# Kernel tuning notes

Hardware: AMD Instinct MI355X
Metric: run time of the kernel (lower is better)

## Reference

```python
import jax, jax.numpy as jnp
import numpy as np

PATCH = 16
HIDDEN = 1024
NUM_HEADS = 16
HEAD_DIM = HIDDEN // NUM_HEADS


def sinusoidal_pe(n, d):
    # standard transformer sinusoidal positional encoding, shape [n, d]
    pos = np.arange(n, dtype=np.float32)[:, None]
    i = np.arange(0, d, 2, dtype=np.float32)[None, :]
    ang = pos / np.power(10000.0, i / d)
    pe = np.zeros((n, d), dtype=np.float32)
    pe[:, 0::2] = np.sin(ang)
    pe[:, 1::2] = np.cos(ang)
    return jnp.asarray(pe)


def patch_embed(x, w, b):
    # Conv2d(kernel=stride=PATCH) == non-overlapping patch GEMM
    B, C, H, W = x.shape
    hp, wp = H // PATCH, W // PATCH
    xp = x.reshape(B, C, hp, PATCH, wp, PATCH)
    t = jnp.einsum('bchpwq,dcpq->bhwd', xp, w)  # [B, hp, wp, D]
    return t.reshape(B, hp * wp, -1) + b        # [B, N, D]


def _fit(x, w, b):
    t = patch_embed(x, w, b)
    t = t + sinusoidal_pe(t.shape[1], t.shape[2])
    B, N, _ = t.shape
    return t.reshape(B, N, NUM_HEADS, HEAD_DIM).transpose(0, 2, 1, 3)  # [B,H,N,hd]


def setup_inputs() -> dict:
    key = jax.random.key(0)
    ks = jax.random.split(key, 9)
    B, C, H, W = 16, 3, 512, 512
    return {
        'q_img': jax.random.normal(ks[0], (B, C, H, W), jnp.float32),
        'k_img': jax.random.normal(ks[1], (B, C, H, W), jnp.float32),
        'v_img': jax.random.normal(ks[2], (B, C, H, W), jnp.float32),
        'wq': jax.random.normal(ks[3], (HIDDEN, C, PATCH, PATCH), jnp.float32) * 0.02,
        'bq': jax.random.normal(ks[4], (HIDDEN,), jnp.float32) * 0.02,
        'wk': jax.random.normal(ks[5], (HIDDEN, C, PATCH, PATCH), jnp.float32) * 0.02,
        'bk': jax.random.normal(ks[6], (HIDDEN,), jnp.float32) * 0.02,
        'wv': jax.random.normal(ks[7], (HIDDEN, C, PATCH, PATCH), jnp.float32) * 0.02,
        'bv': jax.random.normal(ks[8], (HIDDEN,), jnp.float32) * 0.02,
    }


def reference(q_img, k_img, v_img, wq, bq, wk, bk, wv, bv):
    q = _fit(q_img, wq, bq)  # [B,H,N,hd]
    k = _fit(k_img, wk, bk)
    v = _fit(v_img, wv, bv)
    q = jax.nn.softmax(q, axis=-1)   # softmax over head_dim
    k = jax.nn.softmax(k, axis=-2)   # softmax over tokens
    scores = jnp.einsum('bhnd,bhne->bhde', k, v)   # k^T v : [B,H,hd,hd]
    ctx = jnp.einsum('bhnd,bhde->bhne', q, scores)  # [B,H,N,hd]
    B, h, N, hd = ctx.shape
    return ctx.transpose(0, 2, 1, 3).reshape(B, N, h * hd)  # [B,N,hidden]
```

## Files before the change

kernel.cpp:

```cpp
#include <hip/hip_runtime.h>
#include <hip/hip_bf16.h>


typedef float  f32x4  __attribute__((ext_vector_type(4)));
typedef __bf16 bf16x8 __attribute__((ext_vector_type(8)));
typedef __bf16 bf16x4 __attribute__((ext_vector_type(4)));

#define LN10000 9.210340371976184f

__device__ __forceinline__ unsigned short f2bf_bits(float f){
  union { float f; unsigned u; } a; a.f = f;
  unsigned r = a.u + 0x7FFFu + ((a.u >> 16) & 1u);
  return (unsigned short)(r >> 16);
}

__device__ __forceinline__ void gload16(const void* g, void* l){
  __builtin_amdgcn_global_load_lds((__attribute__((address_space(1))) void*)g,
                                   (__attribute__((address_space(3))) void*)l,
                                   16, 0, 0);
}


__global__ __launch_bounds__(256) void k_prep_w(
    const float* __restrict__ wq, const float* __restrict__ wk,
    const float* __restrict__ wv, unsigned short* __restrict__ wbf)
{
  int i = blockIdx.x*256 + threadIdx.x;
  if (i >= 589824) return;
  int z = i / 196608;
  int r = i - z*196608;
  const float* src = (z==0) ? wq : (z==1 ? wk : wv);
  f32x4 v = ((const f32x4*)src)[r];
  unsigned lo = (unsigned)f2bf_bits(v[0]) | ((unsigned)f2bf_bits(v[1]) << 16);
  unsigned hh = (unsigned)f2bf_bits(v[2]) | ((unsigned)f2bf_bits(v[3]) << 16);
  ((uint2*)wbf)[i] = make_uint2(lo, hh);
}

__global__ __launch_bounds__(256) void k_prep_pe(float* __restrict__ pe)
{
  int i = blockIdx.x*256 + threadIdx.x;
  if (i >= 1048576) return;
  int n = i >> 10, dd = i & 1023;
  float ex  = (float)(dd & ~1) * (1.0f/1024.0f);
  float ang = (float)n * expf(-LN10000 * ex);
  pe[i] = (dd & 1) ? cosf(ang) : sinf(ang);
}


__global__ __launch_bounds__(256, 2) void k_embed(
    const float* __restrict__ xq, const float* __restrict__ xk,
    const float* __restrict__ xv, const unsigned short* __restrict__ wbf,
    const float* __restrict__ bq, const float* __restrict__ bk,
    const float* __restrict__ bv, const float* __restrict__ pe,
    unsigned short* __restrict__ t_bf)
{
  __shared__ __align__(16) float          ldsA[128*64];
  __shared__ __align__(16) unsigned short ldsB[128*64];

  const int tid = threadIdx.x;
  int flat = blockIdx.x + (blockIdx.y << 3) + (blockIdx.z << 10);
  int orig = (flat & 7)*384 + (flat >> 3);
  const int z   = orig >> 10;
  const int rem = orig & 1023;
  const int m0  = (rem >> 3) * 128;
  const int d0  = (rem & 7) * 128;

  const float* x = (z==0) ? xq : (z==1 ? xk : xv);
  const unsigned short* wz = wbf + z*786432;
  const float* bias = (z==0) ? bq : (z==1 ? bk : bv);
  unsigned short* tout = t_bf + (size_t)z*16777216u;

  int aRow[8], aKK[8];
#pragma unroll
  for (int i=0;i<8;i++){
    int L   = i*4096 + tid*16;
    int row = L >> 8;
    int U   = L ^ ((row & 7) << 4);
    aKK[i]  = (U >> 2) & 63;
    int m   = m0 + row;
    int bimg = m >> 10, nt = m & 1023;
    aRow[i] = bimg*786432 + (nt>>5)*8192 + (nt&31)*16;
  }
  int bOff[4];
#pragma unroll
  for (int i=0;i<4;i++){
    int L   = i*4096 + tid*16;
    int row = L >> 7;
    int U   = L ^ ((row & 7) << 4);
    bOff[i] = (d0 + row)*768 + ((U >> 1) & 63);
  }

  const int lane = tid & 63;
  const int wid  = tid >> 6;
  const int ln   = lane & 15, hi4 = lane >> 4;
  const int wm   = wid >> 1,  wn  = wid & 1;

  f32x4 acc[4][4] = {};
  char* ldsAc = (char*)ldsA;
  char* ldsBc = (char*)ldsB;

  for (int ks=0; ks<12; ++ks){
#pragma unroll
    for (int i=0;i<8;i++){
      int k   = ks*64 + aKK[i];
      int c   = k >> 8, rem2 = k & 255;
      int goff = aRow[i] + c*262144 + (rem2>>4)*512 + (rem2 & 15);
      gload16(x + goff, ldsAc + i*4096 + wid*1024);
    }
#pragma unroll
    for (int i=0;i<4;i++){
      gload16(wz + bOff[i] + ks*64, ldsBc + i*4096 + wid*1024);
    }
    __syncthreads();

#pragma unroll
    for (int kc=0; kc<2; ++kc){
      bf16x8 af[4], bfr[4];
#pragma unroll
      for (int mi=0;mi<4;mi++){
        int row  = wm*64 + mi*16 + ln;
        int swz  = (row & 7) << 4;
        int base = row*256 + kc*128 + hi4*32;
        f32x4 lo = *(const f32x4*)(ldsAc + ( base        ^ swz));
        f32x4 hh = *(const f32x4*)(ldsAc + ((base + 16)  ^ swz));
        bf16x8 t;
        t[0]=(__bf16)lo[0]; t[1]=(__bf16)lo[1]; t[2]=(__bf16)lo[2]; t[3]=(__bf16)lo[3];
        t[4]=(__bf16)hh[0]; t[5]=(__bf16)hh[1]; t[6]=(__bf16)hh[2]; t[7]=(__bf16)hh[3];
        af[mi] = t;
      }
#pragma unroll
      for (int ni=0;ni<4;ni++){
        int row  = wn*64 + ni*16 + ln;
        int swz  = (row & 7) << 4;
        int base = row*128 + kc*64 + hi4*16;
        bfr[ni] = *(const bf16x8*)(ldsBc + (base ^ swz));
      }
#pragma unroll
      for (int mi=0;mi<4;mi++)
#pragma unroll
        for (int ni=0;ni<4;ni++)
          acc[mi][ni] = __builtin_amdgcn_mfma_f32_16x16x32_bf16(
              af[mi], bfr[ni], acc[mi][ni], 0, 0, 0);
    }
    __syncthreads();
  }

  float bias4[4];
#pragma unroll
  for (int ni=0;ni<4;ni++) bias4[ni] = bias[d0 + wn*64 + ni*16 + ln];

#pragma unroll
  for (int mi=0;mi<4;mi++){
#pragma unroll
    for (int r=0;r<4;r++){
      int m    = m0 + wm*64 + mi*16 + hi4*4 + r;
      int ntok = m & 1023;
      float vv[4];
#pragma unroll
      for (int ni=0;ni<4;ni++){
        int dd = d0 + wn*64 + ni*16 + ln;
        vv[ni] = acc[mi][ni][r] + bias4[ni] + pe[ntok*1024 + dd];
      }
      size_t base = (size_t)m*1024 + d0 + wn*64 + ln;
      if (z == 0){
        float ex0=__expf(vv[0]), ex1=__expf(vv[1]),
              ex2=__expf(vv[2]), ex3=__expf(vv[3]);
        float ps = ex0+ex1+ex2+ex3;
        ps += __shfl_xor(ps, 1); ps += __shfl_xor(ps, 2);
        ps += __shfl_xor(ps, 4); ps += __shfl_xor(ps, 8);
        float w = 1.0f / ps;
        tout[base +  0] = f2bf_bits(ex0*w);  tout[base + 16] = f2bf_bits(ex1*w);
        tout[base + 32] = f2bf_bits(ex2*w);  tout[base + 48] = f2bf_bits(ex3*w);
      } else if (z == 1){
        tout[base +  0] = f2bf_bits(__expf(vv[0]));
        tout[base + 16] = f2bf_bits(__expf(vv[1]));
        tout[base + 32] = f2bf_bits(__expf(vv[2]));
        tout[base + 48] = f2bf_bits(__expf(vv[3]));
      } else {
        tout[base +  0] = f2bf_bits(vv[0]); tout[base + 16] = f2bf_bits(vv[1]);
        tout[base + 32] = f2bf_bits(vv[2]); tout[base + 48] = f2bf_bits(vv[3]);
      }
    }
  }
}


__global__ __launch_bounds__(512) void k_scores(
    const __bf16* __restrict__ t_bf, float* __restrict__ scoresOut)
{
  __shared__ __align__(16) float lds[4][4096];
  __shared__ float ksumLds[8][64];

  const int tid = threadIdx.x;
  const int bh  = blockIdx.x;
  const int b   = bh >> 4, h = bh & 15;
  const __bf16* kbase = t_bf + 16777216u + (size_t)b*1048576u + h*64;
  const __bf16* vbase = t_bf + 33554432u + (size_t)b*1048576u + h*64;

  const int dq = tid & 15, eg = (tid>>4) & 3, npart = tid >> 6;
  const int srow = tid >> 3;
  const int dcol = (tid & 7) * 8;

#define STAGE(BUF, CH) do{                                                \
    size_t g = (size_t)((CH)*64 + srow)*1024 + dcol;                      \
    bf16x8 k8 = *(const bf16x8*)(kbase + g);                              \
    bf16x8 v8 = *(const bf16x8*)(vbase + g);                              \
    f32x4 e0, e1, w0, w1;                                                 \
    e0[0]=(float)k8[0]; e0[1]=(float)k8[1]; e0[2]=(float)k8[2]; e0[3]=(float)k8[3]; \
    e1[0]=(float)k8[4]; e1[1]=(float)k8[5]; e1[2]=(float)k8[6]; e1[3]=(float)k8[7]; \
    w0[0]=(float)v8[0]; w0[1]=(float)v8[1]; w0[2]=(float)v8[2]; w0[3]=(float)v8[3]; \
    w1[0]=(float)v8[4]; w1[1]=(float)v8[5]; w1[2]=(float)v8[6]; w1[3]=(float)v8[7]; \
    *(f32x4*)(&lds[BUF][srow*64 + dcol])       = e0;                      \
    *(f32x4*)(&lds[BUF][srow*64 + dcol + 4])   = e1;                      \
    *(f32x4*)(&lds[2+(BUF)][srow*64 + dcol])     = w0;                    \
    *(f32x4*)(&lds[2+(BUF)][srow*64 + dcol + 4]) = w1;                    \
  }while(0)

  float acc[4][16] = {};
  float kp[4] = {0.f,0.f,0.f,0.f};

  STAGE(0, 0);
  __syncthreads();
  for (int ch=0; ch<16; ++ch){
    int cur = ch & 1;
    if (ch < 15) STAGE(cur^1, ch+1);
    for (int nn = npart; nn < 64; nn += 8){
      f32x4 ek4 = *(const f32x4*)(&lds[cur][nn*64 + dq*4]);
      f32x4 v0  = *(const f32x4*)(&lds[2+cur][nn*64 + eg*16 + 0]);
      f32x4 v1  = *(const f32x4*)(&lds[2+cur][nn*64 + eg*16 + 4]);
      f32x4 v2  = *(const f32x4*)(&lds[2+cur][nn*64 + eg*16 + 8]);
      f32x4 v3  = *(const f32x4*)(&lds[2+cur][nn*64 + eg*16 + 12]);
#pragma unroll
      for (int i2=0;i2<4;i2++){
        kp[i2] += ek4[i2];
#pragma unroll
        for (int j=0;j<4;j++){
          acc[i2][j+0]  += ek4[i2]*v0[j];
          acc[i2][j+4]  += ek4[i2]*v1[j];
          acc[i2][j+8]  += ek4[i2]*v2[j];
          acc[i2][j+12] += ek4[i2]*v3[j];
        }
      }
    }
    __syncthreads();
  }
#undef STAGE

  if (eg == 0){
#pragma unroll
    for (int i2=0;i2<4;i2++) ksumLds[npart][dq*4 + i2] = kp[i2];
  }

  if (npart < 4){
    float* pb = &lds[npart][0];
#pragma unroll
    for (int i2=0;i2<4;i2++){
      int base = (dq*4 + i2)*64 + eg*16;
      f32x4 a0; a0[0]=acc[i2][0];  a0[1]=acc[i2][1];  a0[2]=acc[i2][2];  a0[3]=acc[i2][3];
      f32x4 a1; a1[0]=acc[i2][4];  a1[1]=acc[i2][5];  a1[2]=acc[i2][6];  a1[3]=acc[i2][7];
      f32x4 a2; a2[0]=acc[i2][8];  a2[1]=acc[i2][9];  a2[2]=acc[i2][10]; a2[3]=acc[i2][11];
      f32x4 a3; a3[0]=acc[i2][12]; a3[1]=acc[i2][13]; a3[2]=acc[i2][14]; a3[3]=acc[i2][15];
      *(f32x4*)(pb + base + 0)  = a0;
      *(f32x4*)(pb + base + 4)  = a1;
      *(f32x4*)(pb + base + 8)  = a2;
      *(f32x4*)(pb + base + 12) = a3;
    }
  }
  __syncthreads();
  if (npart >= 4){
    float* pb = &lds[npart-4][0];
#pragma unroll
    for (int i2=0;i2<4;i2++){
      int base = (dq*4 + i2)*64 + eg*16;
#pragma unroll
      for (int q=0;q<4;q++){
        f32x4 cu = *(const f32x4*)(pb + base + 4*q);
        cu[0]+=acc[i2][4*q+0]; cu[1]+=acc[i2][4*q+1];
        cu[2]+=acc[i2][4*q+2]; cu[3]+=acc[i2][4*q+3];
        *(f32x4*)(pb + base + 4*q) = cu;
      }
    }
  }
  __syncthreads();

  float* outp = scoresOut + (size_t)bh*4096;
#pragma unroll
  for (int i=0;i<2;i++){
    int idx = tid + 512*i;
    int q4  = idx*4;
    int d   = idx >> 4;
    float rk = 1.0f / (ksumLds[0][d]+ksumLds[1][d]+ksumLds[2][d]+ksumLds[3][d]
                      +ksumLds[4][d]+ksumLds[5][d]+ksumLds[6][d]+ksumLds[7][d]);
    f32x4 s = *(const f32x4*)(&lds[0][q4]) + *(const f32x4*)(&lds[1][q4])
            + *(const f32x4*)(&lds[2][q4]) + *(const f32x4*)(&lds[3][q4]);
    s[0]*=rk; s[1]*=rk; s[2]*=rk; s[3]*=rk;
    *(f32x4*)(outp + q4) = s;
  }
}


__global__ __launch_bounds__(256) void k_ctx(
    const __bf16* __restrict__ t_bf, const float* __restrict__ scoresIn,
    float* __restrict__ out)
{
  __shared__ __align__(16) float S[64*64];
  __shared__ __align__(16) float qnT[64*132];

  const int tid   = threadIdx.x;
  const int bh    = blockIdx.y;
  const int b     = bh >> 4, h = bh & 15;
  const int chunk = blockIdx.x;
  const __bf16* qbase = t_bf + (size_t)b*1048576u + h*64;

#pragma unroll
  for (int i=0;i<4;i++){
    int q4 = (tid + 256*i)*4;
    *(f32x4*)(S + q4) = *(const f32x4*)(scoresIn + (size_t)bh*4096 + q4);
  }

  const int lane = tid & 63, w = tid >> 6;
  const int pos = lane & 15, rq = lane >> 4;
#pragma unroll
  for (int p=0;p<8;p++){
    int nl = w*32 + p*4 + rq;
    int n  = chunk*128 + nl;
    bf16x4 qv = *(const bf16x4*)(qbase + (size_t)n*1024 + pos*4);
    qnT[(pos*4+0)*132 + nl] = (float)qv[0];
    qnT[(pos*4+1)*132 + nl] = (float)qv[1];
    qnT[(pos*4+2)*132 + nl] = (float)qv[2];
    qnT[(pos*4+3)*132 + nl] = (float)qv[3];
  }
  __syncthreads();

  const int eq = tid & 15, tg = tid >> 4;
  float acc[8][4] = {};
  for (int d=0; d<64; ++d){
    f32x4 s4 = *(const f32x4*)(S   + d*64  + eq*4);
    f32x4 q0 = *(const f32x4*)(qnT + d*132 + tg*8 + 0);
    f32x4 q1 = *(const f32x4*)(qnT + d*132 + tg*8 + 4);
#pragma unroll
    for (int j=0;j<4;j++){
      acc[0][j] += q0[0]*s4[j];
      acc[1][j] += q0[1]*s4[j];
      acc[2][j] += q0[2]*s4[j];
      acc[3][j] += q0[3]*s4[j];
      acc[4][j] += q1[0]*s4[j];
      acc[5][j] += q1[1]*s4[j];
      acc[6][j] += q1[2]*s4[j];
      acc[7][j] += q1[3]*s4[j];
    }
  }
#pragma unroll
  for (int i2=0;i2<8;i2++){
    int n = chunk*128 + tg*8 + i2;
    f32x4 o; o[0]=acc[i2][0]; o[1]=acc[i2][1]; o[2]=acc[i2][2]; o[3]=acc[i2][3];
    *(f32x4*)(out + (size_t)(b*1024 + n)*1024 + h*64 + eq*4) = o;
  }
}


extern "C" void kernel_launch(void* const* d_in, const int* in_sizes, int n_in,
                              void* d_out, int out_size, void* d_ws, size_t ws_size,
                              hipStream_t stream)
{
  const float* q_img = (const float*)d_in[0];
  const float* k_img = (const float*)d_in[1];
  const float* v_img = (const float*)d_in[2];
  const float* wq    = (const float*)d_in[3];
  const float* bq    = (const float*)d_in[4];
  const float* wk    = (const float*)d_in[5];
  const float* bk    = (const float*)d_in[6];
  const float* wv    = (const float*)d_in[7];
  const float* bv    = (const float*)d_in[8];
  float* out = (float*)d_out;
  char*  ws  = (char*)d_ws;

  unsigned short* t_bf   = (unsigned short*)ws;
  unsigned short* wbf    = (unsigned short*)(ws + 0x6000000);
  float*          pe     = (float*)(ws + 0x6480000);
  float*          scores = (float*)(ws + 0x6880000);

  k_prep_w <<<dim3(2304), dim3(256), 0, stream>>>(wq, wk, wv, wbf);
  k_prep_pe<<<dim3(4096), dim3(256), 0, stream>>>(pe);
  k_embed  <<<dim3(8,128,3), dim3(256), 0, stream>>>(q_img,k_img,v_img, wbf,
                                                     bq,bk,bv, pe, t_bf);
  k_scores <<<dim3(256),  dim3(512), 0, stream>>>((const __bf16*)t_bf, scores);
  k_ctx    <<<dim3(8,256), dim3(256), 0, stream>>>((const __bf16*)t_bf, scores, out);
}
```

Measured before the change: 252.1 us.

## Pre-convert input images to bf16 in a separate pass before patch-embed GEMM

Adds a k_prep_x kernel that converts the three fp32 input images to bf16 in the workspace. The embed GEMM then loads bf16 A tiles directly, which halves its A-tile LDS footprint and removes the per-fragment fp32-to-bf16 conversion. Occupancy is raised to 5 blocks per CU. The cost is an extra full read and write pass over the images (about 150MB of traffic) plus one more kernel launch.

```diff
diff --git a/kernel.cpp b/kernel.cpp
--- a/kernel.cpp
+++ b/kernel.cpp
@@ -46,15 +46,34 @@
   pe[i] = (dd & 1) ? cosf(ang) : sinf(ang);
 }
 
-
-__global__ __launch_bounds__(256, 2) void k_embed(
+__global__ __launch_bounds__(256) void k_prep_x(
     const float* __restrict__ xq, const float* __restrict__ xk,
-    const float* __restrict__ xv, const unsigned short* __restrict__ wbf,
+    const float* __restrict__ xv, unsigned short* __restrict__ x_bf)
+{
+  int i = blockIdx.x*256 + threadIdx.x;
+  if (i >= 4718592) return;
+  int z = i / 1572864;
+  int r = i - z*1572864;
+  const float* src = (z==0) ? xq : (z==1 ? xk : xv);
+  f32x4 a = ((const f32x4*)src)[r*2];
+  f32x4 b = ((const f32x4*)src)[r*2+1];
+  uint4 o;
+  o.x = (unsigned)f2bf_bits(a[0]) | ((unsigned)f2bf_bits(a[1]) << 16);
+  o.y = (unsigned)f2bf_bits(a[2]) | ((unsigned)f2bf_bits(a[3]) << 16);
+  o.z = (unsigned)f2bf_bits(b[0]) | ((unsigned)f2bf_bits(b[1]) << 16);
+  o.w = (unsigned)f2bf_bits(b[2]) | ((unsigned)f2bf_bits(b[3]) << 16);
+  ((uint4*)x_bf)[i] = o;
+}
+
+
+__global__ __launch_bounds__(256, 5) void k_embed(
+    const unsigned short* __restrict__ x_bf,
+    const unsigned short* __restrict__ wbf,
     const float* __restrict__ bq, const float* __restrict__ bk,
     const float* __restrict__ bv, const float* __restrict__ pe,
     unsigned short* __restrict__ t_bf)
 {
-  __shared__ __align__(16) float          ldsA[128*64];
+  __shared__ __align__(16) unsigned short ldsA[128*64];
   __shared__ __align__(16) unsigned short ldsB[128*64];
 
   const int tid = threadIdx.x;
@@ -65,21 +84,21 @@
   const int m0  = (rem >> 3) * 128;
   const int d0  = (rem & 7) * 128;
 
-  const float* x = (z==0) ? xq : (z==1 ? xk : xv);
-  const unsigned short* wz = wbf + z*786432;
+  const unsigned short* xbz = x_bf + (size_t)z*12582912u;
+  const unsigned short* wz  = wbf + z*786432;
   const float* bias = (z==0) ? bq : (z==1 ? bk : bv);
   unsigned short* tout = t_bf + (size_t)z*16777216u;
 
-  int aRow[8], aKK[8];
-#pragma unroll
-  for (int i=0;i<8;i++){
+  int aRowG[4], aKK[4];
+#pragma unroll
+  for (int i=0;i<4;i++){
     int L   = i*4096 + tid*16;
-    int row = L >> 8;
+    int row = L >> 7;
     int U   = L ^ ((row & 7) << 4);
-    aKK[i]  = (U >> 2) & 63;
+    aKK[i]  = (U & 127) >> 1;
     int m   = m0 + row;
     int bimg = m >> 10, nt = m & 1023;
-    aRow[i] = bimg*786432 + (nt>>5)*8192 + (nt&31)*16;
+    aRowG[i] = bimg*786432 + (nt>>5)*8192 + (nt&31)*16;
   }
   int bOff[4];
 #pragma unroll
@@ -101,11 +120,11 @@
 
   for (int ks=0; ks<12; ++ks){
 #pragma unroll
-    for (int i=0;i<8;i++){
+    for (int i=0;i<4;i++){
       int k   = ks*64 + aKK[i];
-      int c   = k >> 8, rem2 = k & 255;
-      int goff = aRow[i] + c*262144 + (rem2>>4)*512 + (rem2 & 15);
-      gload16(x + goff, ldsAc + i*4096 + wid*1024);
+      int c   = k >> 8, r2 = k & 255;
+      gload16(xbz + aRowG[i] + c*262144 + (r2>>4)*512 + (r2 & 15),
+              ldsAc + i*4096 + wid*1024);
     }
 #pragma unroll
     for (int i=0;i<4;i++){
@@ -119,21 +138,14 @@
 #pragma unroll
       for (int mi=0;mi<4;mi++){
         int row  = wm*64 + mi*16 + ln;
-        int swz  = (row & 7) << 4;
-        int base = row*256 + kc*128 + hi4*32;
-        f32x4 lo = *(const f32x4*)(ldsAc + ( base        ^ swz));
-        f32x4 hh = *(const f32x4*)(ldsAc + ((base + 16)  ^ swz));
-        bf16x8 t;
-        t[0]=(__bf16)lo[0]; t[1]=(__bf16)lo[1]; t[2]=(__bf16)lo[2]; t[3]=(__bf16)lo[3];
-        t[4]=(__bf16)hh[0]; t[5]=(__bf16)hh[1]; t[6]=(__bf16)hh[2]; t[7]=(__bf16)hh[3];
-        af[mi] = t;
+        int byte = (row*128 + kc*64 + hi4*16) ^ ((row & 7) << 4);
+        af[mi] = *(const bf16x8*)(ldsAc + byte);
       }
 #pragma unroll
       for (int ni=0;ni<4;ni++){
         int row  = wn*64 + ni*16 + ln;
-        int swz  = (row & 7) << 4;
-        int base = row*128 + kc*64 + hi4*16;
-        bfr[ni] = *(const bf16x8*)(ldsBc + (base ^ swz));
+        int byte = (row*128 + kc*64 + hi4*16) ^ ((row & 7) << 4);
+        bfr[ni] = *(const bf16x8*)(ldsBc + byte);
       }
 #pragma unroll
       for (int mi=0;mi<4;mi++)
@@ -379,10 +391,12 @@
   unsigned short* wbf    = (unsigned short*)(ws + 0x6000000);
   float*          pe     = (float*)(ws + 0x6480000);
   float*          scores = (float*)(ws + 0x6880000);
-
-  k_prep_w <<<dim3(2304), dim3(256), 0, stream>>>(wq, wk, wv, wbf);
-  k_prep_pe<<<dim3(4096), dim3(256), 0, stream>>>(pe);
-  k_embed  <<<dim3(8,128,3), dim3(256), 0, stream>>>(q_img,k_img,v_img, wbf,
+  unsigned short* x_bf   = (unsigned short*)(ws + 0x6C80000);
+
+  k_prep_w <<<dim3(2304),  dim3(256), 0, stream>>>(wq, wk, wv, wbf);
+  k_prep_pe<<<dim3(4096),  dim3(256), 0, stream>>>(pe);
+  k_prep_x <<<dim3(18432), dim3(256), 0, stream>>>(q_img, k_img, v_img, x_bf);
+  k_embed  <<<dim3(8,128,3), dim3(256), 0, stream>>>(x_bf, wbf,
                                                      bq,bk,bv, pe, t_bf);
   k_scores <<<dim3(256),  dim3(512), 0, stream>>>((const __bf16*)t_bf, scores);
   k_ctx    <<<dim3(8,256), dim3(256), 0, stream>>>((const __bf16*)t_bf, scores, out);
```

Result: slower. 454.4 us (+80.3%).
